# Kernel optimization log

Hardware: AMD Instinct MI355X
Metric: run time of the kernel (lower is better)

## Reference

```python
import jax, jax.numpy as jnp
import numpy as np
from jax.scipy.special import logsumexp

B, D, T, O = 8, 64, 512, 256  # batch, channels (d_dim), observed timestamps, grid points


def setup_inputs() -> dict:
    key = jax.random.key(0)
    k1, k2, k3 = jax.random.split(key, 3)
    vals = jax.random.normal(k1, (B, D, T), dtype=jnp.float32)
    mask = (jax.random.uniform(k2, (B, D, T)) < 0.7).astype(jnp.float32)
    mask = mask.at[:, :, 0].set(1.0)  # ensure >=1 observation per (b, channel)
    times = jnp.sort(jax.random.uniform(k3, (B, D, T), dtype=jnp.float32), axis=-1)
    x = jnp.concatenate([vals, mask, times], axis=1)  # (B, 3*D, T)
    grid = jnp.broadcast_to(jnp.linspace(0.0, 1.0, O, dtype=jnp.float32), (B, O))
    kernel = jnp.zeros((D,), dtype=jnp.float32)  # learned per-channel log-bandwidth
    return {"x": x, "interpolation_grid": grid, "kernel": kernel}


def reference(x, interpolation_grid, kernel):
    d_dim = kernel.shape[0]
    x_t = x[:, :d_dim]            # (B, D, T) observed values
    m = x[:, d_dim:2 * d_dim]     # (B, D, T) observation mask in {0,1}
    t = x[:, 2 * d_dim:3 * d_dim] # (B, D, T) observation timestamps

    alpha = jax.nn.softplus(kernel)[None, :, None, None]  # pos_kernel, (1,D,1,1)
    # squared distance between observed times and reference grid: (B,D,T,O)
    norm = (t[:, :, :, None] - interpolation_grid[:, None, None, :]) ** 2
    # log(mask): -inf (clamped) where unobserved, 0 where observed
    logm = jnp.log(jnp.maximum(m, 1e-30))[:, :, :, None]

    s = -alpha * norm + logm                      # (B,D,T,O) masked RBF logits
    w = logsumexp(s, axis=2)                      # (B,D,O) intensity channel
    w1 = jnp.exp(s - w[:, :, None, :])            # softmax over T
    y = jnp.sum(w1 * x_t[:, :, :, None], axis=2)  # (B,D,O) smooth interpolation

    s10 = -10.0 * alpha * norm + logm             # sharper kernel (transient)
    wt_lse = logsumexp(s10, axis=2)
    wt = jnp.exp(s10 - wt_lse[:, :, None, :])
    y_trans = jnp.sum(wt * x_t[:, :, :, None], axis=2)  # (B,D,O)

    return jnp.concatenate([y, w, y_trans], axis=1)  # (B, 3*D, O)
```

## Files before the change

kernel.cpp:

```cpp
#include <hip/hip_runtime.h>
#include <math.h>


namespace {
constexpr int kB = 8, kD = 64, kT = 512, kO = 256;
constexpr int kQ = 4;
constexpr int kTH = kO * kQ;
constexpr int kTQ = kT / kQ;
constexpr float kLOG2E = 1.4426950408889634f;
constexpr float kLN2   = 0.6931471805599453f;
}

__global__ __launch_bounds__(kTH, 8) void interp_kernel(
    const float* __restrict__ x,
    const float* __restrict__ grid,
    const float* __restrict__ kern,
    float* __restrict__ out)
{
    __shared__ __align__(16) float smem[4096];
    float* s_u = smem;
    float* s_w = smem + kT;
    float* s_v = smem + 2 * kT;

    const int tid = threadIdx.x;
    const int o   = tid & (kO - 1);
    const int q   = tid >> 8;
    const int bd  = blockIdx.x;
    const int b   = bd >> 6;
    const int d   = bd & (kD - 1);

    const float* base  = x + (size_t)b * (3 * kD * kT);
    const float* vals  = base + (size_t)d * kT;
    const float* mask  = base + (size_t)(kD + d) * kT;
    const float* times = base + (size_t)(2 * kD + d) * kT;

    const float k     = kern[d];
    const float alpha = fmaxf(k, 0.0f) + log1pf(expf(-fabsf(k)));
    const float a2    = alpha * kLOG2E;

    if (tid < kT) {
        const float tt = times[tid];
        const float mm = mask[tid];
        const float lm = __builtin_amdgcn_logf(fmaxf(mm, 1e-30f));
        s_u[tid] = fmaf(-a2 * tt, tt, lm);
        s_w[tid] = 2.0f * a2 * tt;
        s_v[tid] = vals[tid];
    }
    __syncthreads();

    const float g = grid[b * kO + o];
    const float c = -a2 * g * g;

    float l0=0.f,l1=0.f,l2=0.f,l3=0.f;
    float y0=0.f,y1=0.f,y2=0.f,y3=0.f;
    float q0=0.f,q1=0.f,q2=0.f,q3=0.f;
    float z0=0.f,z1=0.f,z2=0.f,z3=0.f;

    const int t0 = q * kTQ;
    #pragma unroll 2
    for (int t = t0; t < t0 + kTQ; t += 4) {
        const float4 uu = *(const float4*)(s_u + t);
        const float4 ww = *(const float4*)(s_w + t);
        const float4 vv = *(const float4*)(s_v + t);

        { float e1 = __builtin_amdgcn_exp2f(fmaf(ww.x, g, uu.x) + c);
          float e2 = e1*e1, e4 = e2*e2, e8 = e4*e4, r = e8*e2;
          l0 += e1; y0 = fmaf(e1, vv.x, y0);
          q0 += r;  z0 = fmaf(r,  vv.x, z0); }
        { float e1 = __builtin_amdgcn_exp2f(fmaf(ww.y, g, uu.y) + c);
          float e2 = e1*e1, e4 = e2*e2, e8 = e4*e4, r = e8*e2;
          l1 += e1; y1 = fmaf(e1, vv.y, y1);
          q1 += r;  z1 = fmaf(r,  vv.y, z1); }
        { float e1 = __builtin_amdgcn_exp2f(fmaf(ww.z, g, uu.z) + c);
          float e2 = e1*e1, e4 = e2*e2, e8 = e4*e4, r = e8*e2;
          l2 += e1; y2 = fmaf(e1, vv.z, y2);
          q2 += r;  z2 = fmaf(r,  vv.z, z2); }
        { float e1 = __builtin_amdgcn_exp2f(fmaf(ww.w, g, uu.w) + c);
          float e2 = e1*e1, e4 = e2*e2, e8 = e4*e4, r = e8*e2;
          l3 += e1; y3 = fmaf(e1, vv.w, y3);
          q3 += r;  z3 = fmaf(r,  vv.w, z3); }
    }

    const float lp = (l0 + l1) + (l2 + l3);
    const float yp = (y0 + y1) + (y2 + y3);
    const float qp = (q0 + q1) + (q2 + q3);
    const float zp = (z0 + z1) + (z2 + z3);

    __syncthreads();
    smem[(q * 4 + 0) * kO + o] = lp;
    smem[(q * 4 + 1) * kO + o] = yp;
    smem[(q * 4 + 2) * kO + o] = qp;
    smem[(q * 4 + 3) * kO + o] = zp;
    __syncthreads();

    if (q == 0) {
        float l = 0.f, ya = 0.f, qs = 0.f, za = 0.f;
        #pragma unroll
        for (int j = 0; j < kQ; ++j) {
            l  += smem[(j * 4 + 0) * kO + o];
            ya += smem[(j * 4 + 1) * kO + o];
            qs += smem[(j * 4 + 2) * kO + o];
            za += smem[(j * 4 + 3) * kO + o];
        }
        const float w = __builtin_amdgcn_logf(l) * kLN2;
        float* ob = out + (size_t)b * (3 * kD * kO);
        ob[(size_t)d * kO + o]            = ya / l;
        ob[(size_t)(kD + d) * kO + o]     = w;
        ob[(size_t)(2 * kD + d) * kO + o] = za / qs;
    }
}

extern "C" void kernel_launch(void* const* d_in, const int* in_sizes, int n_in,
                              void* d_out, int out_size, void* d_ws, size_t ws_size,
                              hipStream_t stream) {
    const float* x    = (const float*)d_in[0];
    const float* grid = (const float*)d_in[1];
    const float* kern = (const float*)d_in[2];
    float* out        = (float*)d_out;
    interp_kernel<<<dim3(kB * kD), dim3(kTH), 0, stream>>>(x, grid, kern, out);
}
```

Before: 77.01 us.

## Split preprocessing into separate kernel and read operands from global memory

Moves the per-timestamp preprocessing (log mask, scaled times) into a separate precompute kernel that writes to workspace. The main kernel then reads U/W/V directly from global memory with scalar loads instead of staging them in shared memory. It also computes the sharp kernel with a second exp2 in place of repeated squaring. This adds a kernel launch, a workspace round trip, a second transcendental per element, and uncoalesced-broadcast global loads in the inner loop.

```diff
diff --git a/kernel.cpp b/kernel.cpp
--- a/kernel.cpp
+++ b/kernel.cpp
@@ -9,18 +9,41 @@
 constexpr int kTQ = kT / kQ;
 constexpr float kLOG2E = 1.4426950408889634f;
 constexpr float kLN2   = 0.6931471805599453f;
+constexpr int kBD = kB * kD;
+constexpr size_t kWsU = 0, kWsW = (size_t)kBD * kT, kWsA2 = 2 * (size_t)kBD * kT;
+}
+
+__global__ __launch_bounds__(kT) void precompute_kernel(
+    const float* __restrict__ x,
+    const float* __restrict__ kern,
+    float* __restrict__ ws)
+{
+    const int bd = blockIdx.x;
+    const int b  = bd >> 6;
+    const int d  = bd & (kD - 1);
+    const int t  = threadIdx.x;
+
+    const float* base  = x + (size_t)b * (3 * kD * kT);
+    const float  mm    = base[(size_t)(kD + d) * kT + t];
+    const float  tt    = base[(size_t)(2 * kD + d) * kT + t];
+
+    const float k     = kern[d];
+    const float alpha = fmaxf(k, 0.0f) + log1pf(expf(-fabsf(k)));
+    const float a2    = alpha * kLOG2E;
+
+    const float lm = __builtin_amdgcn_logf(fmaxf(mm, 1e-30f));
+    ws[kWsU + (size_t)bd * kT + t] = fmaf(-a2 * tt, tt, lm);
+    ws[kWsW + (size_t)bd * kT + t] = 2.0f * a2 * tt;
+    if (t == 0) ws[kWsA2 + bd] = a2;
 }
 
 __global__ __launch_bounds__(kTH, 8) void interp_kernel(
     const float* __restrict__ x,
     const float* __restrict__ grid,
-    const float* __restrict__ kern,
+    const float* __restrict__ ws,
     float* __restrict__ out)
 {
-    __shared__ __align__(16) float smem[4096];
-    float* s_u = smem;
-    float* s_w = smem + kT;
-    float* s_v = smem + 2 * kT;
+    __shared__ float s_part[kQ * 4 * kO];
 
     const int tid = threadIdx.x;
     const int o   = tid & (kO - 1);
@@ -29,78 +52,57 @@
     const int b   = bd >> 6;
     const int d   = bd & (kD - 1);
 
-    const float* base  = x + (size_t)b * (3 * kD * kT);
-    const float* vals  = base + (size_t)d * kT;
-    const float* mask  = base + (size_t)(kD + d) * kT;
-    const float* times = base + (size_t)(2 * kD + d) * kT;
+    const float* __restrict__ U = ws + kWsU + (size_t)bd * kT;
+    const float* __restrict__ W = ws + kWsW + (size_t)bd * kT;
+    const float* __restrict__ V =
+        x + (size_t)b * (3 * kD * kT) + (size_t)d * kT;
 
-    const float k     = kern[d];
-    const float alpha = fmaxf(k, 0.0f) + log1pf(expf(-fabsf(k)));
-    const float a2    = alpha * kLOG2E;
+    const float a2 = ws[kWsA2 + bd];
+    const float g  = grid[b * kO + o];
+    const float c  = -a2 * g * g;
 
-    if (tid < kT) {
-        const float tt = times[tid];
-        const float mm = mask[tid];
-        const float lm = __builtin_amdgcn_logf(fmaxf(mm, 1e-30f));
-        s_u[tid] = fmaf(-a2 * tt, tt, lm);
-        s_w[tid] = 2.0f * a2 * tt;
-        s_v[tid] = vals[tid];
-    }
-    __syncthreads();
-
-    const float g = grid[b * kO + o];
-    const float c = -a2 * g * g;
-
-    float l0=0.f,l1=0.f,l2=0.f,l3=0.f;
-    float y0=0.f,y1=0.f,y2=0.f,y3=0.f;
-    float q0=0.f,q1=0.f,q2=0.f,q3=0.f;
-    float z0=0.f,z1=0.f,z2=0.f,z3=0.f;
+    float l0 = 0.f, l1 = 0.f, y0 = 0.f, y1 = 0.f;
+    float q0 = 0.f, q1 = 0.f, z0 = 0.f, z1 = 0.f;
 
     const int t0 = q * kTQ;
-    #pragma unroll 2
-    for (int t = t0; t < t0 + kTQ; t += 4) {
-        const float4 uu = *(const float4*)(s_u + t);
-        const float4 ww = *(const float4*)(s_w + t);
-        const float4 vv = *(const float4*)(s_v + t);
+    #pragma unroll 4
+    for (int t = t0; t < t0 + kTQ; t += 2) {
+        const float ua = U[t],     ub = U[t + 1];
+        const float wa = W[t],     wb = W[t + 1];
+        const float va = V[t],     vb = V[t + 1];
 
-        { float e1 = __builtin_amdgcn_exp2f(fmaf(ww.x, g, uu.x) + c);
-          float e2 = e1*e1, e4 = e2*e2, e8 = e4*e4, r = e8*e2;
-          l0 += e1; y0 = fmaf(e1, vv.x, y0);
-          q0 += r;  z0 = fmaf(r,  vv.x, z0); }
-        { float e1 = __builtin_amdgcn_exp2f(fmaf(ww.y, g, uu.y) + c);
-          float e2 = e1*e1, e4 = e2*e2, e8 = e4*e4, r = e8*e2;
-          l1 += e1; y1 = fmaf(e1, vv.y, y1);
-          q1 += r;  z1 = fmaf(r,  vv.y, z1); }
-        { float e1 = __builtin_amdgcn_exp2f(fmaf(ww.z, g, uu.z) + c);
-          float e2 = e1*e1, e4 = e2*e2, e8 = e4*e4, r = e8*e2;
-          l2 += e1; y2 = fmaf(e1, vv.z, y2);
-          q2 += r;  z2 = fmaf(r,  vv.z, z2); }
-        { float e1 = __builtin_amdgcn_exp2f(fmaf(ww.w, g, uu.w) + c);
-          float e2 = e1*e1, e4 = e2*e2, e8 = e4*e4, r = e8*e2;
-          l3 += e1; y3 = fmaf(e1, vv.w, y3);
-          q3 += r;  z3 = fmaf(r,  vv.w, z3); }
+        float arg_a = ua + c;
+        arg_a = fmaf(wa, g, arg_a);
+        float e1a  = __builtin_amdgcn_exp2f(arg_a);
+        float e10a = __builtin_amdgcn_exp2f(10.0f * arg_a);
+        l0 += e1a;  y0 = fmaf(e1a,  va, y0);
+        q0 += e10a; z0 = fmaf(e10a, va, z0);
+
+        float arg_b = ub + c;
+        arg_b = fmaf(wb, g, arg_b);
+        float e1b  = __builtin_amdgcn_exp2f(arg_b);
+        float e10b = __builtin_amdgcn_exp2f(10.0f * arg_b);
+        l1 += e1b;  y1 = fmaf(e1b,  vb, y1);
+        q1 += e10b; z1 = fmaf(e10b, vb, z1);
     }
 
-    const float lp = (l0 + l1) + (l2 + l3);
-    const float yp = (y0 + y1) + (y2 + y3);
-    const float qp = (q0 + q1) + (q2 + q3);
-    const float zp = (z0 + z1) + (z2 + z3);
+    const float lp = l0 + l1, yp = y0 + y1;
+    const float qp = q0 + q1, zp = z0 + z1;
 
-    __syncthreads();
-    smem[(q * 4 + 0) * kO + o] = lp;
-    smem[(q * 4 + 1) * kO + o] = yp;
-    smem[(q * 4 + 2) * kO + o] = qp;
-    smem[(q * 4 + 3) * kO + o] = zp;
+    s_part[(q * 4 + 0) * kO + o] = lp;
+    s_part[(q * 4 + 1) * kO + o] = yp;
+    s_part[(q * 4 + 2) * kO + o] = qp;
+    s_part[(q * 4 + 3) * kO + o] = zp;
     __syncthreads();
 
     if (q == 0) {
         float l = 0.f, ya = 0.f, qs = 0.f, za = 0.f;
         #pragma unroll
         for (int j = 0; j < kQ; ++j) {
-            l  += smem[(j * 4 + 0) * kO + o];
-            ya += smem[(j * 4 + 1) * kO + o];
-            qs += smem[(j * 4 + 2) * kO + o];
-            za += smem[(j * 4 + 3) * kO + o];
+            l  += s_part[(j * 4 + 0) * kO + o];
+            ya += s_part[(j * 4 + 1) * kO + o];
+            qs += s_part[(j * 4 + 2) * kO + o];
+            za += s_part[(j * 4 + 3) * kO + o];
         }
         const float w = __builtin_amdgcn_logf(l) * kLN2;
         float* ob = out + (size_t)b * (3 * kD * kO);
@@ -117,5 +119,8 @@
     const float* grid = (const float*)d_in[1];
     const float* kern = (const float*)d_in[2];
     float* out        = (float*)d_out;
-    interp_kernel<<<dim3(kB * kD), dim3(kTH), 0, stream>>>(x, grid, kern, out);
+    float* ws         = (float*)d_ws;
+
+    precompute_kernel<<<dim3(kBD), dim3(kT), 0, stream>>>(x, kern, ws);
+    interp_kernel<<<dim3(kBD), dim3(kTH), 0, stream>>>(x, grid, ws, out);
 }
```

Result: slower. 83.39 us (+8.3%).
